# Kernel optimization log

Hardware: AMD Instinct MI355X
Metric: run time of the kernel (lower is better)

Reference implementation:

```python
import jax, jax.numpy as jnp
import numpy as np

B, N, D = 1, 1024, 3584
H, KVH, HD = 28, 4, 128
I = 18944
SEC = [16, 24, 24]  # mrope_section, sums to HD//2
EPS_RMS = 1e-6
EPS_SM = 1e-6


def setup_inputs() -> dict:
    key = jax.random.key(0)
    ks = jax.random.split(key, 16)
    s = 0.02
    return {
        "hidden_states": jax.random.normal(ks[0], (B, N, D), jnp.float32),
        "cos": jax.random.uniform(ks[1], (3, B, N, HD), jnp.float32, -1.0, 1.0),
        "sin": jax.random.uniform(ks[2], (3, B, N, HD), jnp.float32, -1.0, 1.0),
        "prune_mask": jax.random.randint(ks[3], (B, N), 0, 2, jnp.int32),
        "Wq": jax.random.normal(ks[4], (D, H * HD), jnp.float32) * s,
        "bq": jnp.zeros((H * HD,), jnp.float32),
        "Wk": jax.random.normal(ks[5], (D, KVH * HD), jnp.float32) * s,
        "bk": jnp.zeros((KVH * HD,), jnp.float32),
        "Wv": jax.random.normal(ks[6], (D, KVH * HD), jnp.float32) * s,
        "bv": jnp.zeros((KVH * HD,), jnp.float32),
        "Wo": jax.random.normal(ks[7], (H * HD, D), jnp.float32) * s,
        "ln1_w": jnp.ones((D,), jnp.float32),
        "ln2_w": jnp.ones((D,), jnp.float32),
        "Wg": jax.random.normal(ks[8], (D, I), jnp.float32) * s,
        "Wu": jax.random.normal(ks[9], (D, I), jnp.float32) * s,
        "Wd": jax.random.normal(ks[10], (I, D), jnp.float32) * s,
    }


def _rmsnorm(x, w):
    v = jnp.mean(x * x, axis=-1, keepdims=True)
    return x * jax.lax.rsqrt(v + EPS_RMS) * w


def _rotate_half(x):
    h = x.shape[-1] // 2
    return jnp.concatenate([-x[..., h:], x[..., :h]], axis=-1)


def _mrope_select(t):
    # t: (3, B, N, HD) -> (B, 1, N, HD), picking section i from axis i%3
    parts, idx = [], 0
    for i, s in enumerate(SEC * 2):
        parts.append(t[i % 3, :, :, idx:idx + s])
        idx += s
    return jnp.concatenate(parts, axis=-1)[:, None]


def reference(hidden_states, cos, sin, prune_mask, Wq, bq, Wk, bk, Wv, bv, Wo,
              ln1_w, ln2_w, Wg, Wu, Wd):
    x = _rmsnorm(hidden_states, ln1_w)
    q = (x @ Wq + bq).reshape(B, N, H, HD).transpose(0, 2, 1, 3)
    k = (x @ Wk + bk).reshape(B, N, KVH, HD).transpose(0, 2, 1, 3)
    v = (x @ Wv + bv).reshape(B, N, KVH, HD).transpose(0, 2, 1, 3)

    cf, sf = _mrope_select(cos), _mrope_select(sin)
    q = q * cf + _rotate_half(q) * sf
    k = k * cf + _rotate_half(k) * sf

    groups = H // KVH
    k = jnp.repeat(k, groups, axis=1)  # (B,H,N,HD)
    v = jnp.repeat(v, groups, axis=1)

    scores = jnp.einsum("bhqd,bhkd->bhqk", q, k) / np.sqrt(HD).astype(np.float32)
    causal = jnp.tril(jnp.ones((N, N), bool))
    scores = jnp.where(causal, scores, jnp.float32(-1e9))

    # custom prune-masked softmax (softmax_with_mask)
    am = prune_mask.astype(jnp.float32)[:, None, None, :]  # (B,1,1,N)
    eye = jnp.eye(N, dtype=jnp.float32)
    am = am + (1.0 - am) * eye
    mx = jnp.max(scores, axis=-1, keepdims=True)
    e = jnp.exp(scores - mx) * am
    attn = (e + EPS_SM / N) / (jnp.sum(e, axis=-1, keepdims=True) + EPS_SM)

    o = jnp.einsum("bhqk,bhkd->bhqd", attn, v)
    o = o.transpose(0, 2, 1, 3).reshape(B, N, H * HD) @ Wo

    h = hidden_states + o
    y = _rmsnorm(h, ln2_w)
    mlp = (jax.nn.silu(y @ Wg) * (y @ Wu)) @ Wd
    return h + mlp
```

## Files before the change

kernel.cpp:

```cpp
#include <hip/hip_runtime.h>
#include <hip/hip_bf16.h>


#define SEQ   1024
#define DIM   3584
#define NH    28
#define NKVH  4
#define HDIM  128
#define IDIM  18944
#define QKVN  4608
#define GUN   37888

typedef __attribute__((ext_vector_type(8))) __bf16 bf16x8;
typedef __attribute__((ext_vector_type(4))) __bf16 bf16x4;
typedef __attribute__((ext_vector_type(4))) float  f32x4;

static constexpr size_t OFF_WQKVT = 0;
static constexpr size_t OFF_WOT   = OFF_WQKVT + (size_t)QKVN*DIM*2;
static constexpr size_t OFF_WGUT  = OFF_WOT   + (size_t)DIM*DIM*2;
static constexpr size_t OFF_WDT   = OFF_WGUT  + (size_t)GUN*DIM*2;
static constexpr size_t OFF_XB    = OFF_WDT   + (size_t)DIM*IDIM*2;
static constexpr size_t OFF_QKV   = OFF_XB    + (size_t)SEQ*DIM*2;
static constexpr size_t OFF_VT    = OFF_QKV   + (size_t)SEQ*QKVN*2;
static constexpr size_t OFF_VSUMP = OFF_VT    + (size_t)NKVH*HDIM*SEQ*2;
static constexpr size_t OFF_VSUM  = OFF_VSUMP + 4*8*128*4;
static constexpr size_t OFF_BQKV  = OFF_VSUM  + 4*128*4;
static constexpr size_t OFF_OB    = OFF_BQKV  + (size_t)QKVN*4;
static constexpr size_t OFF_HB    = OFF_OB    + (size_t)SEQ*DIM*2;
static constexpr size_t OFF_YB    = OFF_HB    + (size_t)SEQ*DIM*4;
static constexpr size_t OFF_GU    = OFF_YB    + (size_t)SEQ*DIM*2;
static constexpr size_t OFF_PB    = OFF_GU    + (size_t)SEQ*GUN*2;
static constexpr size_t OFF_PART  = OFF_GU;

#define GLL16(gp, lp)                                                        \
  __builtin_amdgcn_global_load_lds(                                         \
      (const __attribute__((address_space(1))) void*)(gp),                  \
      (__attribute__((address_space(3))) void*)(lp), 16, 0, 0)

#define BAR    asm volatile("s_barrier" ::: "memory")
#define LGKM0  asm volatile("s_waitcnt lgkmcnt(0)" ::: "memory")
#define VM4    asm volatile("s_waitcnt vmcnt(4)" ::: "memory")

__global__ __launch_bounds__(256) void transconv_kernel(
    const float* __restrict__ W, __bf16* __restrict__ WT, int K, int N, int mode)
{
  __shared__ __bf16 t[64][72];
  const int tid = threadIdx.x;
  const int k0 = blockIdx.y * 64, n0 = blockIdx.x * 64;
#pragma unroll
  for (int it = 0; it < 4; ++it) {
    int idx = it * 256 + tid;
    int r = idx >> 4, c4 = idx & 15;
    float4 v = *(const float4*)(W + (size_t)(k0 + r) * N + n0 + c4 * 4);
    t[r][c4 * 4 + 0] = (__bf16)v.x;
    t[r][c4 * 4 + 1] = (__bf16)v.y;
    t[r][c4 * 4 + 2] = (__bf16)v.z;
    t[r][c4 * 4 + 3] = (__bf16)v.w;
  }
  __syncthreads();
#pragma unroll
  for (int it = 0; it < 2; ++it) {
    int idx = it * 256 + tid;
    int r = idx >> 3, c8 = idx & 7;
    bf16x8 o;
#pragma unroll
    for (int i = 0; i < 8; ++i) o[i] = t[c8 * 8 + i][r];
    const int nlog = n0 + r;
    const int orow = (mode == 0) ? nlog
                   : ((nlog >> 4) << 5) + ((mode == 2) ? 16 : 0) + (nlog & 15);
    *(bf16x8*)(WT + (size_t)orow * K + k0 + c8 * 8) = o;
  }
}

__global__ __launch_bounds__(256) void pack_bias_kernel(
    const float* __restrict__ bq, const float* __restrict__ bk,
    const float* __restrict__ bv, float* __restrict__ out)
{
  int i = blockIdx.x * 256 + threadIdx.x;
  if (i < DIM) out[i] = bq[i];
  else if (i < DIM + 512) out[i] = bk[i - DIM];
  else if (i < QKVN) out[i] = bv[i - DIM - 512];
}

__global__ __launch_bounds__(256) void rmsnorm_kernel(
    const float* __restrict__ in, const float* __restrict__ w,
    __bf16* __restrict__ out)
{
  const int row = blockIdx.x;
  const int t = threadIdx.x;
  const float* x = in + (size_t)row * DIM;
  float4 v[4];
  float ss = 0.f;
#pragma unroll
  for (int i = 0; i < 4; ++i) {
    int idx = t + i * 256;
    if (idx < 896) {
      v[i] = ((const float4*)x)[idx];
      ss += v[i].x * v[i].x + v[i].y * v[i].y + v[i].z * v[i].z + v[i].w * v[i].w;
    }
  }
#pragma unroll
  for (int m = 1; m < 64; m <<= 1) ss += __shfl_xor(ss, m);
  __shared__ float red[4];
  if ((t & 63) == 0) red[t >> 6] = ss;
  __syncthreads();
  float tot = red[0] + red[1] + red[2] + red[3];
  float rs = rsqrtf(tot / (float)DIM + 1e-6f);
#pragma unroll
  for (int i = 0; i < 4; ++i) {
    int idx = t + i * 256;
    if (idx < 896) {
      float4 wv = ((const float4*)w)[idx];
      bf16x4 o;
      o[0] = (__bf16)(v[i].x * rs * wv.x);
      o[1] = (__bf16)(v[i].y * rs * wv.y);
      o[2] = (__bf16)(v[i].z * rs * wv.z);
      o[3] = (__bf16)(v[i].w * rs * wv.w);
      *(bf16x4*)(out + (size_t)row * DIM + idx * 4) = o;
    }
  }
}

template<int S, bool BF16OUT, bool BIAS>
__global__ __launch_bounds__(256) void reduce_kernel(
    const float* __restrict__ part, const float* __restrict__ resid,
    const float* __restrict__ bias, void* __restrict__ out, int N, int MN4)
{
  const int i4 = blockIdx.x * 256 + threadIdx.x;
  if (i4 >= MN4) return;
  const size_t base = (size_t)i4 * 4;
  f32x4 s = *(const f32x4*)(part + base);
#pragma unroll
  for (int k = 1; k < S; ++k)
    s += *(const f32x4*)(part + (size_t)k * MN4 * 4 + base);
  if (BIAS) {
    const int col = (int)(base % N);
    s += *(const f32x4*)(bias + col);
  }
  if (resid != nullptr) s += *(const f32x4*)(resid + base);
  if (BF16OUT) {
    bf16x4 o;
#pragma unroll
    for (int j = 0; j < 4; ++j) o[j] = (__bf16)s[j];
    *(bf16x4*)((__bf16*)out + base) = o;
  } else {
    *(f32x4*)((float*)out + base) = s;
  }
}

template<int EPI>
__global__ __launch_bounds__(512, 1) void gemm256_kernel(
    const __bf16* __restrict__ A, const __bf16* __restrict__ BT,
    void* __restrict__ OUT, int M, int N, int K, int Kc, int gridY)
{
  __shared__ int4 lds4[8192];
  char* ldsc = (char*)lds4;
  const int tid = threadIdx.x;
  const int l = tid & 63, w = tid >> 6;
  const int wr = w >> 2, wc = w & 3;
  const int lg = l >> 4, lc = l & 15;

  const int nwg = gridDim.x;
  const int bq8 = nwg >> 3, br8 = nwg & 7;
  const int xcd = blockIdx.x & 7, bidx = blockIdx.x >> 3;
  const int wg = (xcd < br8 ? xcd * (bq8 + 1) : br8 * (bq8 + 1) + (xcd - br8) * bq8) + bidx;
  const int ntn = N >> 8;
  const int wg2 = wg / gridY;
  const int row0 = (wg % gridY) * 256;
  const int col0 = (wg2 % ntn) * 256;
  const int ks = wg2 / ntn;
  const int kbase = ks * Kc;

  size_t aoffj[2], boffj[2];
  int dstj[2];
#pragma unroll
  for (int j = 0; j < 2; ++j) {
    const int c = (j * 8 + w) * 64 + l;
    const int r = c >> 3, p = c & 7;
    const int b = p ^ (r & 7);
    aoffj[j] = (size_t)(row0 + r) * K + kbase + b * 8;
    boffj[j] = (size_t)(col0 + r) * K + kbase + b * 8;
    dstj[j] = (j * 8 + w) * 1024;
  }

#define STG_A(U, KT, BUFB) do {                                              \
    GLL16(A + aoffj[0] + (size_t)(U) * 128 * K + (size_t)(KT) * 64,          \
          ldsc + (BUFB) + (U) * 16384 + dstj[0]);                            \
    GLL16(A + aoffj[1] + (size_t)(U) * 128 * K + (size_t)(KT) * 64,          \
          ldsc + (BUFB) + (U) * 16384 + dstj[1]); } while (0)
#define STG_B(U, KT, BUFB) do {                                              \
    GLL16(BT + boffj[0] + (size_t)(U) * 128 * K + (size_t)(KT) * 64,         \
          ldsc + (BUFB) + 32768 + (U) * 16384 + dstj[0]);                    \
    GLL16(BT + boffj[1] + (size_t)(U) * 128 * K + (size_t)(KT) * 64,         \
          ldsc + (BUFB) + 32768 + (U) * 16384 + dstj[1]); } while (0)

  const int sw = lc & 7;
  const int rdA = (wr * 128 + lc) * 128;
  const int rdB = 32768 + (wc * 64 + lc) * 128;
  const int sk0 = (lg ^ sw) * 16;
  const int sk1 = ((4 | lg) ^ sw) * 16;

  f32x4 acc[8][4] = {};
  bf16x8 af[4][2], bfr[4][2];

#define RD_A4(MH, BUFB) do { _Pragma("unroll")                               \
    for (int mm = 0; mm < 4; ++mm) {                                         \
      af[mm][0] = *(const bf16x8*)(ldsc + (BUFB) + rdA + ((MH) * 4 + mm) * 2048 + sk0); \
      af[mm][1] = *(const bf16x8*)(ldsc + (BUFB) + rdA + ((MH) * 4 + mm) * 2048 + sk1); } } while (0)
#define RD_B2(NL, BUFB) do { _Pragma("unroll")                               \
    for (int nn = 0; nn < 2; ++nn) {                                         \
      bfr[(NL) + nn][0] = *(const bf16x8*)(ldsc + (BUFB) + rdB + ((NL) + nn) * 2048 + sk0); \
      bfr[(NL) + nn][1] = *(const bf16x8*)(ldsc + (BUFB) + rdB + ((NL) + nn) * 2048 + sk1); } } while (0)

#define MFMA16(MH, NL) do { _Pragma("unroll")                                \
    for (int mm = 0; mm < 4; ++mm) { _Pragma("unroll")                       \
      for (int nn = 0; nn < 2; ++nn) {                                       \
        acc[(MH)*4+mm][(NL)+nn] = __builtin_amdgcn_mfma_f32_16x16x32_bf16(   \
            af[mm][0], bfr[(NL)+nn][0], acc[(MH)*4+mm][(NL)+nn], 0, 0, 0);   \
        acc[(MH)*4+mm][(NL)+nn] = __builtin_amdgcn_mfma_f32_16x16x32_bf16(   \
            af[mm][1], bfr[(NL)+nn][1], acc[(MH)*4+mm][(NL)+nn], 0, 0, 0); } } } while (0)

#define DO_MFMA(MH, NL)                                                      \
    __builtin_amdgcn_s_setprio(1); MFMA16(MH, NL);                           \
    __builtin_amdgcn_s_setprio(0)

  STG_B(0, 0, 0); STG_B(1, 0, 0); STG_A(0, 0, 0); STG_A(1, 0, 0);
  STG_B(0, 1, 65536); STG_B(1, 1, 65536);
  VM4;
  BAR;

  const int T = Kc >> 6;
#pragma unroll 1
  for (int i = 0; i < (T >> 1); ++i) {
    const int t1 = 2 * i + 1;
    const int se = (2 * i + 2 < T) ? 2 * i + 2 : 2 * i;
    const int so = (2 * i + 3 < T) ? 2 * i + 3 : t1;
    RD_A4(0, 0); RD_B2(0, 0); STG_A(0, t1, 65536);
    BAR; LGKM0; DO_MFMA(0, 0); BAR;
    RD_B2(2, 0); STG_A(1, t1, 65536);
    BAR; LGKM0; DO_MFMA(0, 2); BAR;
    RD_A4(1, 0); STG_B(0, se, 0);
    BAR; LGKM0; DO_MFMA(1, 2); BAR;
    STG_B(1, se, 0);
    VM4;
    BAR; DO_MFMA(1, 0); BAR;
    RD_A4(0, 65536); RD_B2(0, 65536); STG_A(0, se, 0);
    BAR; LGKM0; DO_MFMA(0, 0); BAR;
    RD_B2(2, 65536); STG_A(1, se, 0);
    BAR; LGKM0; DO_MFMA(0, 2); BAR;
    RD_A4(1, 65536); STG_B(0, so, 65536);
    BAR; LGKM0; DO_MFMA(1, 2); BAR;
    STG_B(1, so, 65536);
    VM4;
    BAR; DO_MFMA(1, 0); BAR;
  }
  asm volatile("s_waitcnt vmcnt(0)" ::: "memory");

  if (EPI == 0) {
    __bf16* PBo = (__bf16*)OUT;
    const int id = N >> 1;
    const int baseq = (col0 + wc * 64) >> 5;
#pragma unroll
    for (int m = 0; m < 8; ++m) {
#pragma unroll
      for (int p = 0; p < 2; ++p) {
        const int gcol = (baseq + p) * 16 + lc;
#pragma unroll
        for (int j = 0; j < 4; ++j) {
          const int row = row0 + wr * 128 + m * 16 + lg * 4 + j;
          const float g = acc[m][2 * p][j];
          const float u = acc[m][2 * p + 1][j];
          const float s = g / (1.f + __expf(-g));
          PBo[(size_t)row * id + gcol] = (__bf16)(s * u);
        }
      }
    }
  } else {
    float* P = (float*)OUT + (size_t)ks * M * N;
#pragma unroll
    for (int m = 0; m < 8; ++m)
#pragma unroll
      for (int n = 0; n < 4; ++n)
#pragma unroll
        for (int j = 0; j < 4; ++j)
          P[(size_t)(row0 + wr * 128 + m * 16 + lg * 4 + j) * N
            + (col0 + wc * 64 + n * 16 + lc)] = acc[m][n][j];
  }
#undef STG_A
#undef STG_B
#undef RD_A4
#undef RD_B2
#undef MFMA16
#undef DO_MFMA
}

__global__ __launch_bounds__(256) void rope_kernel(
    __bf16* __restrict__ qkv, const float* __restrict__ cosb,
    const float* __restrict__ sinb)
{
  const int n = blockIdx.x;
  for (int p = threadIdx.x; p < 32 * 64; p += 256) {
    const int head = p >> 6;
    const int d = p & 63;
    const int src = (d < 16) ? 0 : (d < 40) ? 1 : 2;
    const float* cb = cosb + (size_t)src * SEQ * HDIM + (size_t)n * HDIM;
    const float* sb = sinb + (size_t)src * SEQ * HDIM + (size_t)n * HDIM;
    const float c0 = cb[d], c1 = cb[d + 64];
    const float s0 = sb[d], s1 = sb[d + 64];
    const int col = (head < NH) ? head * HDIM : DIM + (head - NH) * HDIM;
    __bf16* q = qkv + (size_t)n * QKVN + col;
    const float a = (float)q[d];
    const float b = (float)q[d + 64];
    q[d]      = (__bf16)(a * c0 - b * s0);
    q[d + 64] = (__bf16)(b * c1 + a * s1);
  }
}

__global__ __launch_bounds__(256) void vtrans_kernel(
    const __bf16* __restrict__ qkv, __bf16* __restrict__ vT,
    float* __restrict__ vsump)
{
  __shared__ __bf16 t[128][132];
  const int nt = blockIdx.x, kvh = blockIdx.y;
  const int n0 = nt * 128;
  const int tid = threadIdx.x;
#pragma unroll
  for (int it = 0; it < 8; ++it) {
    int idx = it * 256 + tid;
    int nl = idx >> 4, c8 = idx & 15;
    bf16x8 v = *(const bf16x8*)(qkv + (size_t)(n0 + nl) * QKVN + 4096 + kvh * HDIM + c8 * 8);
#pragma unroll
    for (int i = 0; i < 8; ++i) t[nl][c8 * 8 + i] = v[i];
  }
  __syncthreads();
#pragma unroll
  for (int it = 0; it < 8; ++it) {
    int idx = it * 256 + tid;
    int d = idx >> 4, c8 = idx & 15;
    bf16x8 o;
#pragma unroll
    for (int i = 0; i < 8; ++i) o[i] = t[c8 * 8 + i][d];
    *(bf16x8*)(vT + (size_t)(kvh * HDIM + d) * SEQ + n0 + c8 * 8) = o;
  }
  if (tid < 128) {
    float s = 0.f;
    for (int nl = 0; nl < 128; ++nl) s += (float)t[nl][tid];
    vsump[(size_t)(kvh * 8 + nt) * 128 + tid] = s;
  }
}

__global__ __launch_bounds__(512) void vsum_reduce_kernel(
    const float* __restrict__ vsump, float* __restrict__ vsum)
{
  const int idx = threadIdx.x;
  const int kvh = idx >> 7, d = idx & 127;
  float s = 0.f;
#pragma unroll
  for (int nt = 0; nt < 8; ++nt) s += vsump[(size_t)(kvh * 8 + nt) * 128 + d];
  vsum[idx] = s;
}

__global__ __launch_bounds__(256) void attn_kernel(
    const __bf16* __restrict__ qkv, const __bf16* __restrict__ vT,
    const float* __restrict__ vsum, const int* __restrict__ prune,
    __bf16* __restrict__ o)
{
  __shared__ __bf16 plds[4 * 16 * 40];
  const int tid = threadIdx.x;
  const int l = tid & 63, w = tid >> 6;
  const int h = blockIdx.y;
  const int kvh = h / 7;
  const int qt = blockIdx.x;
  const int qbase = qt * 64 + w * 16;
  const int lg = l >> 4, lc = l & 15;
  __bf16* pw = plds + w * (16 * 40);

  bf16x8 qf[4];
#pragma unroll
  for (int s = 0; s < 4; ++s)
    qf[s] = *(const bf16x8*)(qkv + (size_t)(qbase + lc) * QKVN + h * HDIM + s * 32 + lg * 8);

  f32x4 oacc[8] = {};
  float mrun[4] = {-3e38f, -3e38f, -3e38f, -3e38f};
  float lrun[4] = {0.f, 0.f, 0.f, 0.f};

  const int kbEnd = ((qbase + 15) >> 5) + 1;
  for (int kb = 0; kb < kbEnd; ++kb) {
    f32x4 sacc[2] = {};
#pragma unroll
    for (int s = 0; s < 4; ++s) {
#pragma unroll
      for (int c = 0; c < 2; ++c) {
        bf16x8 kf = *(const bf16x8*)(qkv + (size_t)(kb * 32 + c * 16 + lc) * QKVN
                                     + DIM + kvh * HDIM + s * 32 + lg * 8);
        sacc[c] = __builtin_amdgcn_mfma_f32_16x16x32_bf16(qf[s], kf, sacc[c], 0, 0, 0);
      }
    }
    float p[2][4];
    int am[2];
#pragma unroll
    for (int c = 0; c < 2; ++c) {
      const int col = kb * 32 + c * 16 + lc;
      am[c] = (prune[col] != 0) ? 1 : 0;
#pragma unroll
      for (int j = 0; j < 4; ++j) {
        const int row = qbase + lg * 4 + j;
        float sv = sacc[c][j] * 0.08838834764831845f;
        p[c][j] = (col <= row) ? sv : -3e38f;
      }
    }
#pragma unroll
    for (int j = 0; j < 4; ++j) {
      float mx = fmaxf(p[0][j], p[1][j]);
      mx = fmaxf(mx, __shfl_xor(mx, 1));
      mx = fmaxf(mx, __shfl_xor(mx, 2));
      mx = fmaxf(mx, __shfl_xor(mx, 4));
      mx = fmaxf(mx, __shfl_xor(mx, 8));
      const float mnew = fmaxf(mrun[j], mx);
      const float scale = __expf(mrun[j] - mnew);
      mrun[j] = mnew;
      const int row = qbase + lg * 4 + j;
      float rs = 0.f;
#pragma unroll
      for (int c = 0; c < 2; ++c) {
        const int col = kb * 32 + c * 16 + lc;
        float e = __expf(p[c][j] - mnew);
        const int keep = (col == row) ? 1 : am[c];
        e = keep ? e : 0.f;
        p[c][j] = e;
        rs += e;
      }
      rs += __shfl_xor(rs, 1);
      rs += __shfl_xor(rs, 2);
      rs += __shfl_xor(rs, 4);
      rs += __shfl_xor(rs, 8);
      lrun[j] = lrun[j] * scale + rs;
#pragma unroll
      for (int df = 0; df < 8; ++df) oacc[df][j] *= scale;
    }
#pragma unroll
    for (int c = 0; c < 2; ++c)
#pragma unroll
      for (int j = 0; j < 4; ++j)
        pw[(lg * 4 + j) * 40 + c * 16 + lc] = (__bf16)p[c][j];
    bf16x8 pa = *(const bf16x8*)(pw + lc * 40 + lg * 8);
#pragma unroll
    for (int df = 0; df < 8; ++df) {
      bf16x8 vf = *(const bf16x8*)(vT + (size_t)(kvh * HDIM + df * 16 + lc) * SEQ + kb * 32 + lg * 8);
      oacc[df] = __builtin_amdgcn_mfma_f32_16x16x32_bf16(pa, vf, oacc[df], 0, 0, 0);
    }
  }
#pragma unroll
  for (int df = 0; df < 8; ++df) {
    const float vs = vsum[kvh * HDIM + df * 16 + lc];
#pragma unroll
    for (int j = 0; j < 4; ++j) {
      const int row = qbase + lg * 4 + j;
      const float denom = lrun[j] + 1e-6f;
      const float val = (oacc[df][j] + 9.765625e-10f * vs) / denom;
      o[(size_t)row * DIM + h * HDIM + df * 16 + lc] = (__bf16)val;
    }
  }
}

extern "C" void kernel_launch(void* const* d_in, const int* in_sizes, int n_in,
                              void* d_out, int out_size, void* d_ws, size_t ws_size,
                              hipStream_t stream) {
  const float* hidden = (const float*)d_in[0];
  const float* cosb   = (const float*)d_in[1];
  const float* sinb   = (const float*)d_in[2];
  const int*   prune  = (const int*)d_in[3];
  const float* Wq     = (const float*)d_in[4];
  const float* bq     = (const float*)d_in[5];
  const float* Wk     = (const float*)d_in[6];
  const float* bk     = (const float*)d_in[7];
  const float* Wv     = (const float*)d_in[8];
  const float* bv     = (const float*)d_in[9];
  const float* Wo     = (const float*)d_in[10];
  const float* ln1    = (const float*)d_in[11];
  const float* ln2    = (const float*)d_in[12];
  const float* Wg     = (const float*)d_in[13];
  const float* Wu     = (const float*)d_in[14];
  const float* Wd     = (const float*)d_in[15];
  float* out = (float*)d_out;
  char* ws = (char*)d_ws;

  __bf16* WQKVT = (__bf16*)(ws + OFF_WQKVT);
  __bf16* WOT   = (__bf16*)(ws + OFF_WOT);
  __bf16* WGUT  = (__bf16*)(ws + OFF_WGUT);
  __bf16* WDT   = (__bf16*)(ws + OFF_WDT);
  __bf16* XB    = (__bf16*)(ws + OFF_XB);
  __bf16* QKV   = (__bf16*)(ws + OFF_QKV);
  __bf16* VT    = (__bf16*)(ws + OFF_VT);
  float*  VSUMP = (float*)(ws + OFF_VSUMP);
  float*  VSUM  = (float*)(ws + OFF_VSUM);
  float*  BQKV  = (float*)(ws + OFF_BQKV);
  __bf16* OB    = (__bf16*)(ws + OFF_OB);
  float*  HB    = (float*)(ws + OFF_HB);
  __bf16* YB    = (__bf16*)(ws + OFF_YB);
  __bf16* PB    = (__bf16*)(ws + OFF_PB);
  float*  PART  = (float*)(ws + OFF_PART);

  transconv_kernel<<<dim3(DIM / 64, DIM / 64), 256, 0, stream>>>(Wq, WQKVT, DIM, DIM, 0);
  transconv_kernel<<<dim3(512 / 64, DIM / 64), 256, 0, stream>>>(Wk, WQKVT + (size_t)DIM * DIM, DIM, 512, 0);
  transconv_kernel<<<dim3(512 / 64, DIM / 64), 256, 0, stream>>>(Wv, WQKVT + (size_t)4096 * DIM, DIM, 512, 0);
  pack_bias_kernel<<<QKVN / 256, 256, 0, stream>>>(bq, bk, bv, BQKV);
  rmsnorm_kernel<<<SEQ, 256, 0, stream>>>(hidden, ln1, XB);

  gemm256_kernel<1><<<(SEQ / 256) * (QKVN / 256) * 2, 512, 0, stream>>>(
      XB, WQKVT, PART, SEQ, QKVN, DIM, DIM / 2, SEQ / 256);
  reduce_kernel<2, true, true><<<(SEQ * QKVN / 4 + 255) / 256, 256, 0, stream>>>(
      PART, nullptr, BQKV, QKV, QKVN, SEQ * QKVN / 4);

  rope_kernel<<<SEQ, 256, 0, stream>>>(QKV, cosb, sinb);
  vtrans_kernel<<<dim3(8, NKVH), 256, 0, stream>>>(QKV, VT, VSUMP);
  vsum_reduce_kernel<<<1, 512, 0, stream>>>(VSUMP, VSUM);
  attn_kernel<<<dim3(SEQ / 64, NH), 256, 0, stream>>>(QKV, VT, VSUM, prune, OB);

  transconv_kernel<<<dim3(DIM / 64, DIM / 64), 256, 0, stream>>>(Wo, WOT, DIM, DIM, 0);
  gemm256_kernel<1><<<(DIM / 256) * (SEQ / 256) * 4, 512, 0, stream>>>(
      OB, WOT, PART, SEQ, DIM, DIM, DIM / 4, SEQ / 256);
  reduce_kernel<4, false, false><<<(SEQ * DIM / 4 + 255) / 256, 256, 0, stream>>>(
      PART, hidden, nullptr, HB, DIM, SEQ * DIM / 4);

  rmsnorm_kernel<<<SEQ, 256, 0, stream>>>(HB, ln2, YB);

  transconv_kernel<<<dim3(IDIM / 64, DIM / 64), 256, 0, stream>>>(Wg, WGUT, DIM, IDIM, 1);
  transconv_kernel<<<dim3(IDIM / 64, DIM / 64), 256, 0, stream>>>(Wu, WGUT, DIM, IDIM, 2);
  gemm256_kernel<0><<<(GUN / 256) * (SEQ / 256), 512, 0, stream>>>(
      YB, WGUT, PB, SEQ, GUN, DIM, DIM, SEQ / 256);

  transconv_kernel<<<dim3(DIM / 64, IDIM / 64), 256, 0, stream>>>(Wd, WDT, IDIM, DIM, 0);
  gemm256_kernel<1><<<(DIM / 256) * (SEQ / 256) * 4, 512, 0, stream>>>(
      PB, WDT, PART, SEQ, DIM, IDIM, IDIM / 4, SEQ / 256);
  reduce_kernel<4, false, false><<<(SEQ * DIM / 4 + 255) / 256, 256, 0, stream>>>(
      PART, HB, nullptr, out, DIM, SEQ * DIM / 4);
}
```

Before: 938.1 us.

## Switch GEMM to 32x32x16 MFMA tiles and fuse split-K reduce with RMSNorm

Changes the 256x256 GEMM inner loop from 16x16x32 MFMAs to 32x32x16 MFMAs. The fragment layout, LDS read pattern and both epilogues are reworked to match, and the SiLU*up pairing now uses a lane shuffle. Launch bounds are raised to allow two workgroups per CU. A new fused kernel sums the O-projection split-K partials with the residual, then computes RMSNorm and writes the bf16 output, replacing two separate kernels. The larger MFMA shape is meant to cut LDS reads per flop. The risks are register pressure under the new launch bound and less efficient strided epilogue stores.

```diff
diff --git a/kernel.cpp b/kernel.cpp
--- a/kernel.cpp
+++ b/kernel.cpp
@@ -11,9 +11,10 @@
 #define QKVN  4608
 #define GUN   37888
 
-typedef __attribute__((ext_vector_type(8))) __bf16 bf16x8;
-typedef __attribute__((ext_vector_type(4))) __bf16 bf16x4;
-typedef __attribute__((ext_vector_type(4))) float  f32x4;
+typedef __attribute__((ext_vector_type(8)))  __bf16 bf16x8;
+typedef __attribute__((ext_vector_type(4)))  __bf16 bf16x4;
+typedef __attribute__((ext_vector_type(4)))  float  f32x4;
+typedef __attribute__((ext_vector_type(16))) float  f32x16;
 
 static constexpr size_t OFF_WQKVT = 0;
 static constexpr size_t OFF_WOT   = OFF_WQKVT + (size_t)QKVN*DIM*2;
@@ -148,8 +149,53 @@
   }
 }
 
+__global__ __launch_bounds__(256) void reduce_rms_kernel(
+    const float* __restrict__ part, const float* __restrict__ resid,
+    const float* __restrict__ w, float* __restrict__ hout,
+    __bf16* __restrict__ yout)
+{
+  const int row = blockIdx.x;
+  const int t = threadIdx.x;
+  const size_t base = (size_t)row * DIM;
+  const size_t slab = (size_t)SEQ * DIM;
+  f32x4 v[4];
+  float ss = 0.f;
+#pragma unroll
+  for (int i = 0; i < 4; ++i) {
+    int idx = t + i * 256;
+    if (idx < 896) {
+      f32x4 s = *(const f32x4*)(part + base + idx * 4);
+      s += *(const f32x4*)(part + slab + base + idx * 4);
+      s += *(const f32x4*)(part + 2 * slab + base + idx * 4);
+      s += *(const f32x4*)(part + 3 * slab + base + idx * 4);
+      s += *(const f32x4*)(resid + base + idx * 4);
+      v[i] = s;
+      ss += s[0] * s[0] + s[1] * s[1] + s[2] * s[2] + s[3] * s[3];
+      *(f32x4*)(hout + base + idx * 4) = s;
+    }
+  }
+#pragma unroll
+  for (int m = 1; m < 64; m <<= 1) ss += __shfl_xor(ss, m);
+  __shared__ float red[4];
+  if ((t & 63) == 0) red[t >> 6] = ss;
+  __syncthreads();
+  float tot = red[0] + red[1] + red[2] + red[3];
+  float rs = rsqrtf(tot / (float)DIM + 1e-6f);
+#pragma unroll
+  for (int i = 0; i < 4; ++i) {
+    int idx = t + i * 256;
+    if (idx < 896) {
+      f32x4 wv = *(const f32x4*)(w + idx * 4);
+      bf16x4 o;
+#pragma unroll
+      for (int j = 0; j < 4; ++j) o[j] = (__bf16)(v[i][j] * rs * wv[j]);
+      *(bf16x4*)(yout + base + idx * 4) = o;
+    }
+  }
+}
+
 template<int EPI>
-__global__ __launch_bounds__(512, 1) void gemm256_kernel(
+__global__ __launch_bounds__(512, 2) void gemm256_kernel(
     const __bf16* __restrict__ A, const __bf16* __restrict__ BT,
     void* __restrict__ OUT, int M, int N, int K, int Kc, int gridY)
 {
@@ -158,7 +204,7 @@
   const int tid = threadIdx.x;
   const int l = tid & 63, w = tid >> 6;
   const int wr = w >> 2, wc = w & 3;
-  const int lg = l >> 4, lc = l & 15;
+  const int l31 = l & 31, oct = l >> 5;
 
   const int nwg = gridDim.x;
   const int bq8 = nwg >> 3, br8 = nwg & 7;
@@ -168,8 +214,8 @@
   const int wg2 = wg / gridY;
   const int row0 = (wg % gridY) * 256;
   const int col0 = (wg2 % ntn) * 256;
-  const int ks = wg2 / ntn;
-  const int kbase = ks * Kc;
+  const int ks_ = wg2 / ntn;
+  const int kbase = ks_ * Kc;
 
   size_t aoffj[2], boffj[2];
   int dstj[2];
@@ -194,34 +240,33 @@
     GLL16(BT + boffj[1] + (size_t)(U) * 128 * K + (size_t)(KT) * 64,         \
           ldsc + (BUFB) + 32768 + (U) * 16384 + dstj[1]); } while (0)
 
-  const int sw = lc & 7;
-  const int rdA = (wr * 128 + lc) * 128;
-  const int rdB = 32768 + (wc * 64 + lc) * 128;
-  const int sk0 = (lg ^ sw) * 16;
-  const int sk1 = ((4 | lg) ^ sw) * 16;
-
-  f32x4 acc[8][4] = {};
-  bf16x8 af[4][2], bfr[4][2];
-
-#define RD_A4(MH, BUFB) do { _Pragma("unroll")                               \
-    for (int mm = 0; mm < 4; ++mm) {                                         \
-      af[mm][0] = *(const bf16x8*)(ldsc + (BUFB) + rdA + ((MH) * 4 + mm) * 2048 + sk0); \
-      af[mm][1] = *(const bf16x8*)(ldsc + (BUFB) + rdA + ((MH) * 4 + mm) * 2048 + sk1); } } while (0)
-#define RD_B2(NL, BUFB) do { _Pragma("unroll")                               \
-    for (int nn = 0; nn < 2; ++nn) {                                         \
-      bfr[(NL) + nn][0] = *(const bf16x8*)(ldsc + (BUFB) + rdB + ((NL) + nn) * 2048 + sk0); \
-      bfr[(NL) + nn][1] = *(const bf16x8*)(ldsc + (BUFB) + rdB + ((NL) + nn) * 2048 + sk1); } } while (0)
-
-#define MFMA16(MH, NL) do { _Pragma("unroll")                                \
-    for (int mm = 0; mm < 4; ++mm) { _Pragma("unroll")                       \
-      for (int nn = 0; nn < 2; ++nn) {                                       \
-        acc[(MH)*4+mm][(NL)+nn] = __builtin_amdgcn_mfma_f32_16x16x32_bf16(   \
-            af[mm][0], bfr[(NL)+nn][0], acc[(MH)*4+mm][(NL)+nn], 0, 0, 0);   \
-        acc[(MH)*4+mm][(NL)+nn] = __builtin_amdgcn_mfma_f32_16x16x32_bf16(   \
-            af[mm][1], bfr[(NL)+nn][1], acc[(MH)*4+mm][(NL)+nn], 0, 0, 0); } } } while (0)
+  const int rbA = (wr * 128 + l31) * 128;
+  const int rbB = 32768 + (wc * 64 + l31) * 128;
+  int sk[4];
+#pragma unroll
+  for (int ks = 0; ks < 4; ++ks) sk[ks] = ((ks * 2 + oct) ^ (l & 7)) * 16;
+
+  f32x16 acc[4][2] = {};
+  bf16x8 af[2][4], bfr[2][4];
+
+#define RD_A2(MH, BUFB) do { _Pragma("unroll")                               \
+    for (int mm = 0; mm < 2; ++mm) { _Pragma("unroll")                       \
+      for (int ks = 0; ks < 4; ++ks)                                         \
+        af[mm][ks] = *(const bf16x8*)(ldsc + (BUFB) + rbA                    \
+            + ((MH) * 2 + mm) * 4096 + sk[ks]); } } while (0)
+#define RD_B4(NL, BUFB) do { _Pragma("unroll")                               \
+    for (int ks = 0; ks < 4; ++ks)                                           \
+      bfr[NL][ks] = *(const bf16x8*)(ldsc + (BUFB) + rbB                     \
+          + (NL) * 4096 + sk[ks]); } while (0)
+
+#define MFMA8(MH, NL) do { _Pragma("unroll")                                 \
+    for (int ks = 0; ks < 4; ++ks) { _Pragma("unroll")                       \
+      for (int mm = 0; mm < 2; ++mm)                                         \
+        acc[(MH)*2+mm][NL] = __builtin_amdgcn_mfma_f32_32x32x16_bf16(        \
+            af[mm][ks], bfr[NL][ks], acc[(MH)*2+mm][NL], 0, 0, 0); } } while (0)
 
 #define DO_MFMA(MH, NL)                                                      \
-    __builtin_amdgcn_s_setprio(1); MFMA16(MH, NL);                           \
+    __builtin_amdgcn_s_setprio(1); MFMA8(MH, NL);                            \
     __builtin_amdgcn_s_setprio(0)
 
   STG_B(0, 0, 0); STG_B(1, 0, 0); STG_A(0, 0, 0); STG_A(1, 0, 0);
@@ -233,64 +278,68 @@
 #pragma unroll 1
   for (int i = 0; i < (T >> 1); ++i) {
     const int t1 = 2 * i + 1;
-    const int se = (2 * i + 2 < T) ? 2 * i + 2 : 2 * i;
+    const int se = (2 * i + 2 < T) ? 2 * i + 2 : 0;
     const int so = (2 * i + 3 < T) ? 2 * i + 3 : t1;
-    RD_A4(0, 0); RD_B2(0, 0); STG_A(0, t1, 65536);
+    RD_A2(0, 0); RD_B4(0, 0); STG_A(0, t1, 65536);
     BAR; LGKM0; DO_MFMA(0, 0); BAR;
-    RD_B2(2, 0); STG_A(1, t1, 65536);
-    BAR; LGKM0; DO_MFMA(0, 2); BAR;
-    RD_A4(1, 0); STG_B(0, se, 0);
-    BAR; LGKM0; DO_MFMA(1, 2); BAR;
+    RD_B4(1, 0); STG_A(1, t1, 65536);
+    BAR; LGKM0; DO_MFMA(0, 1); BAR;
+    RD_A2(1, 0); STG_B(0, se, 0);
+    BAR; LGKM0; DO_MFMA(1, 0); BAR;
     STG_B(1, se, 0);
     VM4;
-    BAR; DO_MFMA(1, 0); BAR;
-    RD_A4(0, 65536); RD_B2(0, 65536); STG_A(0, se, 0);
+    BAR; DO_MFMA(1, 1); BAR;
+    RD_A2(0, 65536); RD_B4(0, 65536); STG_A(0, se, 0);
     BAR; LGKM0; DO_MFMA(0, 0); BAR;
-    RD_B2(2, 65536); STG_A(1, se, 0);
-    BAR; LGKM0; DO_MFMA(0, 2); BAR;
-    RD_A4(1, 65536); STG_B(0, so, 65536);
-    BAR; LGKM0; DO_MFMA(1, 2); BAR;
+    RD_B4(1, 65536); STG_A(1, se, 0);
+    BAR; LGKM0; DO_MFMA(0, 1); BAR;
+    RD_A2(1, 65536); STG_B(0, so, 65536);
+    BAR; LGKM0; DO_MFMA(1, 0); BAR;
     STG_B(1, so, 65536);
     VM4;
-    BAR; DO_MFMA(1, 0); BAR;
+    BAR; DO_MFMA(1, 1); BAR;
   }
   asm volatile("s_waitcnt vmcnt(0)" ::: "memory");
 
   if (EPI == 0) {
     __bf16* PBo = (__bf16*)OUT;
     const int id = N >> 1;
-    const int baseq = (col0 + wc * 64) >> 5;
-#pragma unroll
-    for (int m = 0; m < 8; ++m) {
-#pragma unroll
-      for (int p = 0; p < 2; ++p) {
-        const int gcol = (baseq + p) * 16 + lc;
-#pragma unroll
-        for (int j = 0; j < 4; ++j) {
-          const int row = row0 + wr * 128 + m * 16 + lg * 4 + j;
-          const float g = acc[m][2 * p][j];
-          const float u = acc[m][2 * p + 1][j];
-          const float s = g / (1.f + __expf(-g));
-          PBo[(size_t)row * id + gcol] = (__bf16)(s * u);
+#pragma unroll
+    for (int m = 0; m < 4; ++m) {
+#pragma unroll
+      for (int n = 0; n < 2; ++n) {
+        const int q = (col0 + wc * 64 + n * 32) >> 5;
+#pragma unroll
+        for (int reg = 0; reg < 16; ++reg) {
+          const int row = row0 + wr * 128 + m * 32
+                        + (reg & 3) + 8 * (reg >> 2) + 4 * oct;
+          const float g = acc[m][n][reg];
+          const float u = __shfl_xor(g, 16);
+          if (l31 < 16) {
+            const float s = g / (1.f + __expf(-g));
+            PBo[(size_t)row * id + q * 16 + (l & 15)] = (__bf16)(s * u);
+          }
         }
       }
     }
   } else {
-    float* P = (float*)OUT + (size_t)ks * M * N;
-#pragma unroll
-    for (int m = 0; m < 8; ++m)
-#pragma unroll
-      for (int n = 0; n < 4; ++n)
-#pragma unroll
-        for (int j = 0; j < 4; ++j)
-          P[(size_t)(row0 + wr * 128 + m * 16 + lg * 4 + j) * N
-            + (col0 + wc * 64 + n * 16 + lc)] = acc[m][n][j];
+    float* P = (float*)OUT + (size_t)ks_ * M * N;
+#pragma unroll
+    for (int m = 0; m < 4; ++m)
+#pragma unroll
+      for (int n = 0; n < 2; ++n)
+#pragma unroll
+        for (int reg = 0; reg < 16; ++reg) {
+          const int row = row0 + wr * 128 + m * 32
+                        + (reg & 3) + 8 * (reg >> 2) + 4 * oct;
+          P[(size_t)row * N + col0 + wc * 64 + n * 32 + l31] = acc[m][n][reg];
+        }
   }
 #undef STG_A
 #undef STG_B
-#undef RD_A4
-#undef RD_B2
-#undef MFMA16
+#undef RD_A2
+#undef RD_B4
+#undef MFMA8
 #undef DO_MFMA
 }
 
@@ -520,10 +569,7 @@
   transconv_kernel<<<dim3(DIM / 64, DIM / 64), 256, 0, stream>>>(Wo, WOT, DIM, DIM, 0);
   gemm256_kernel<1><<<(DIM / 256) * (SEQ / 256) * 4, 512, 0, stream>>>(
       OB, WOT, PART, SEQ, DIM, DIM, DIM / 4, SEQ / 256);
-  reduce_kernel<4, false, false><<<(SEQ * DIM / 4 + 255) / 256, 256, 0, stream>>>(
-      PART, hidden, nullptr, HB, DIM, SEQ * DIM / 4);
-
-  rmsnorm_kernel<<<SEQ, 256, 0, stream>>>(HB, ln2, YB);
+  reduce_rms_kernel<<<SEQ, 256, 0, stream>>>(PART, hidden, ln2, HB, YB);
 
   transconv_kernel<<<dim3(IDIM / 64, DIM / 64), 256, 0, stream>>>(Wg, WGUT, DIM, IDIM, 1);
   transconv_kernel<<<dim3(IDIM / 64, DIM / 64), 256, 0, stream>>>(Wu, WGUT, DIM, IDIM, 2);
```

Measured after the change: 1.021 ms. +8.8%, slower.

## Persist gate/up GEMM with atomic tile scheduler and fuse reduce with RMSNorm

Applied to the files above, without the earlier changes.

The gate/up GEMM now runs as a persistent kernel with 256 workgroups that take 256x256 output tiles from a global atomic counter. Before, it launched one workgroup per tile. The counter is reset inside a new fused kernel that sums the O-projection split-K partials, adds the residual, and applies the second RMSNorm in one pass, replacing a separate reduce and a separate rmsnorm launch. The goal is to cut the tail-wave imbalance across 592 tiles and save one launch plus one read and write of HB. The cost is an atomic and a barrier per tile, and the loss of the XCD-aware tile ordering in the persistent path, which may reduce L2 locality.

```diff
diff --git a/kernel.cpp b/kernel.cpp
--- a/kernel.cpp
+++ b/kernel.cpp
@@ -31,6 +31,7 @@
 static constexpr size_t OFF_GU    = OFF_YB    + (size_t)SEQ*DIM*2;
 static constexpr size_t OFF_PB    = OFF_GU    + (size_t)SEQ*GUN*2;
 static constexpr size_t OFF_PART  = OFF_GU;
+static constexpr size_t OFF_CTR   = OFF_VSUMP;
 
 #define GLL16(gp, lp)                                                        \
   __builtin_amdgcn_global_load_lds(                                         \
@@ -148,40 +149,108 @@
   }
 }
 
-template<int EPI>
+__global__ __launch_bounds__(256) void reduce_rms_kernel(
+    const float* __restrict__ part, const float* __restrict__ resid,
+    const float* __restrict__ w, float* __restrict__ hout,
+    __bf16* __restrict__ yout, int* __restrict__ ctr)
+{
+  const int row = blockIdx.x;
+  const int t = threadIdx.x;
+  if (row == 0 && t == 0) atomicExch(ctr, 0);
+  const size_t base = (size_t)row * DIM;
+  const size_t slab = (size_t)SEQ * DIM;
+  f32x4 v[4];
+  float ss = 0.f;
+#pragma unroll
+  for (int i = 0; i < 4; ++i) {
+    int idx = t + i * 256;
+    if (idx < 896) {
+      f32x4 s = *(const f32x4*)(part + base + idx * 4);
+      s += *(const f32x4*)(part + slab + base + idx * 4);
+      s += *(const f32x4*)(part + 2 * slab + base + idx * 4);
+      s += *(const f32x4*)(part + 3 * slab + base + idx * 4);
+      s += *(const f32x4*)(resid + base + idx * 4);
+      v[i] = s;
+      ss += s[0] * s[0] + s[1] * s[1] + s[2] * s[2] + s[3] * s[3];
+      *(f32x4*)(hout + base + idx * 4) = s;
+    }
+  }
+#pragma unroll
+  for (int m = 1; m < 64; m <<= 1) ss += __shfl_xor(ss, m);
+  __shared__ float red[4];
+  if ((t & 63) == 0) red[t >> 6] = ss;
+  __syncthreads();
+  float tot = red[0] + red[1] + red[2] + red[3];
+  float rs = rsqrtf(tot / (float)DIM + 1e-6f);
+#pragma unroll
+  for (int i = 0; i < 4; ++i) {
+    int idx = t + i * 256;
+    if (idx < 896) {
+      f32x4 wv = *(const f32x4*)(w + idx * 4);
+      bf16x4 o;
+#pragma unroll
+      for (int j = 0; j < 4; ++j) o[j] = (__bf16)(v[i][j] * rs * wv[j]);
+      *(bf16x4*)(yout + base + idx * 4) = o;
+    }
+  }
+}
+
+template<int EPI, int PERSIST>
 __global__ __launch_bounds__(512, 1) void gemm256_kernel(
     const __bf16* __restrict__ A, const __bf16* __restrict__ BT,
-    void* __restrict__ OUT, int M, int N, int K, int Kc, int gridY)
+    void* __restrict__ OUT, int M, int N, int K, int Kc, int gridY,
+    int NT, int* __restrict__ ctr)
 {
   __shared__ int4 lds4[8192];
+  __shared__ int s_t;
   char* ldsc = (char*)lds4;
   const int tid = threadIdx.x;
   const int l = tid & 63, w = tid >> 6;
   const int wr = w >> 2, wc = w & 3;
   const int lg = l >> 4, lc = l & 15;
 
-  const int nwg = gridDim.x;
-  const int bq8 = nwg >> 3, br8 = nwg & 7;
-  const int xcd = blockIdx.x & 7, bidx = blockIdx.x >> 3;
-  const int wg = (xcd < br8 ? xcd * (bq8 + 1) : br8 * (bq8 + 1) + (xcd - br8) * bq8) + bidx;
-  const int ntn = N >> 8;
-  const int wg2 = wg / gridY;
-  const int row0 = (wg % gridY) * 256;
-  const int col0 = (wg2 % ntn) * 256;
-  const int ks = wg2 / ntn;
-  const int kbase = ks * Kc;
-
-  size_t aoffj[2], boffj[2];
-  int dstj[2];
+  int cdst[2], crow[2], cslot[2];
 #pragma unroll
   for (int j = 0; j < 2; ++j) {
     const int c = (j * 8 + w) * 64 + l;
-    const int r = c >> 3, p = c & 7;
-    const int b = p ^ (r & 7);
-    aoffj[j] = (size_t)(row0 + r) * K + kbase + b * 8;
-    boffj[j] = (size_t)(col0 + r) * K + kbase + b * 8;
-    dstj[j] = (j * 8 + w) * 1024;
-  }
+    crow[j] = c >> 3;
+    cslot[j] = (c & 7) ^ (crow[j] & 7);
+    cdst[j] = (j * 8 + w) * 1024;
+  }
+  const int sw = lc & 7;
+  const int rdA = (wr * 128 + lc) * 128;
+  const int rdB = 32768 + (wc * 64 + lc) * 128;
+  const int sk0 = (lg ^ sw) * 16;
+  const int sk1 = ((4 | lg) ^ sw) * 16;
+  const int ntn = N >> 8;
+
+  for (;;) {
+    int tw;
+    if (PERSIST) {
+      if (tid == 0) s_t = atomicAdd(ctr, 1);
+      __syncthreads();
+      tw = s_t;
+      if (tw >= NT) return;
+    } else {
+      const int nwg = gridDim.x;
+      const int bq8 = nwg >> 3, br8 = nwg & 7;
+      const int xcd = blockIdx.x & 7, bidx = blockIdx.x >> 3;
+      tw = (xcd < br8 ? xcd * (bq8 + 1) : br8 * (bq8 + 1) + (xcd - br8) * bq8) + bidx;
+    }
+    const int wg2 = tw / gridY;
+    const int row0 = (tw % gridY) * 256;
+    const int col0 = (wg2 % ntn) * 256;
+    const int ks_ = wg2 / ntn;
+    const int kbase = ks_ * Kc;
+
+    size_t aoffj[2], boffj[2];
+    int dstj[2];
+#pragma unroll
+    for (int j = 0; j < 2; ++j) {
+      aoffj[j] = (size_t)(row0 + crow[j]) * K + kbase + cslot[j] * 8;
+      boffj[j] = (size_t)(col0 + crow[j]) * K + kbase + cslot[j] * 8;
+      dstj[j] = cdst[j];
+    }
 
 #define STG_A(U, KT, BUFB) do {                                              \
     GLL16(A + aoffj[0] + (size_t)(U) * 128 * K + (size_t)(KT) * 64,          \
@@ -194,14 +263,8 @@
     GLL16(BT + boffj[1] + (size_t)(U) * 128 * K + (size_t)(KT) * 64,         \
           ldsc + (BUFB) + 32768 + (U) * 16384 + dstj[1]); } while (0)
 
-  const int sw = lc & 7;
-  const int rdA = (wr * 128 + lc) * 128;
-  const int rdB = 32768 + (wc * 64 + lc) * 128;
-  const int sk0 = (lg ^ sw) * 16;
-  const int sk1 = ((4 | lg) ^ sw) * 16;
-
-  f32x4 acc[8][4] = {};
-  bf16x8 af[4][2], bfr[4][2];
+    f32x4 acc[8][4] = {};
+    bf16x8 af[4][2], bfr[4][2];
 
 #define RD_A4(MH, BUFB) do { _Pragma("unroll")                               \
     for (int mm = 0; mm < 4; ++mm) {                                         \
@@ -224,67 +287,69 @@
     __builtin_amdgcn_s_setprio(1); MFMA16(MH, NL);                           \
     __builtin_amdgcn_s_setprio(0)
 
-  STG_B(0, 0, 0); STG_B(1, 0, 0); STG_A(0, 0, 0); STG_A(1, 0, 0);
-  STG_B(0, 1, 65536); STG_B(1, 1, 65536);
-  VM4;
-  BAR;
-
-  const int T = Kc >> 6;
+    STG_B(0, 0, 0); STG_B(1, 0, 0); STG_A(0, 0, 0); STG_A(1, 0, 0);
+    STG_B(0, 1, 65536); STG_B(1, 1, 65536);
+    VM4;
+    BAR;
+
+    const int T = Kc >> 6;
 #pragma unroll 1
-  for (int i = 0; i < (T >> 1); ++i) {
-    const int t1 = 2 * i + 1;
-    const int se = (2 * i + 2 < T) ? 2 * i + 2 : 2 * i;
-    const int so = (2 * i + 3 < T) ? 2 * i + 3 : t1;
-    RD_A4(0, 0); RD_B2(0, 0); STG_A(0, t1, 65536);
-    BAR; LGKM0; DO_MFMA(0, 0); BAR;
-    RD_B2(2, 0); STG_A(1, t1, 65536);
-    BAR; LGKM0; DO_MFMA(0, 2); BAR;
-    RD_A4(1, 0); STG_B(0, se, 0);
-    BAR; LGKM0; DO_MFMA(1, 2); BAR;
-    STG_B(1, se, 0);
-    VM4;
-    BAR; DO_MFMA(1, 0); BAR;
-    RD_A4(0, 65536); RD_B2(0, 65536); STG_A(0, se, 0);
-    BAR; LGKM0; DO_MFMA(0, 0); BAR;
-    RD_B2(2, 65536); STG_A(1, se, 0);
-    BAR; LGKM0; DO_MFMA(0, 2); BAR;
-    RD_A4(1, 65536); STG_B(0, so, 65536);
-    BAR; LGKM0; DO_MFMA(1, 2); BAR;
-    STG_B(1, so, 65536);
-    VM4;
-    BAR; DO_MFMA(1, 0); BAR;
-  }
-  asm volatile("s_waitcnt vmcnt(0)" ::: "memory");
-
-  if (EPI == 0) {
-    __bf16* PBo = (__bf16*)OUT;
-    const int id = N >> 1;
-    const int baseq = (col0 + wc * 64) >> 5;
-#pragma unroll
-    for (int m = 0; m < 8; ++m) {
-#pragma unroll
-      for (int p = 0; p < 2; ++p) {
-        const int gcol = (baseq + p) * 16 + lc;
-#pragma unroll
-        for (int j = 0; j < 4; ++j) {
-          const int row = row0 + wr * 128 + m * 16 + lg * 4 + j;
-          const float g = acc[m][2 * p][j];
-          const float u = acc[m][2 * p + 1][j];
-          const float s = g / (1.f + __expf(-g));
-          PBo[(size_t)row * id + gcol] = (__bf16)(s * u);
+    for (int i = 0; i < (T >> 1); ++i) {
+      const int t1 = 2 * i + 1;
+      const int se = (2 * i + 2 < T) ? 2 * i + 2 : 2 * i;
+      const int so = (2 * i + 3 < T) ? 2 * i + 3 : t1;
+      RD_A4(0, 0); RD_B2(0, 0); STG_A(0, t1, 65536);
+      BAR; LGKM0; DO_MFMA(0, 0); BAR;
+      RD_B2(2, 0); STG_A(1, t1, 65536);
+      BAR; LGKM0; DO_MFMA(0, 2); BAR;
+      RD_A4(1, 0); STG_B(0, se, 0);
+      BAR; LGKM0; DO_MFMA(1, 2); BAR;
+      STG_B(1, se, 0);
+      VM4;
+      BAR; DO_MFMA(1, 0); BAR;
+      RD_A4(0, 65536); RD_B2(0, 65536); STG_A(0, se, 0);
+      BAR; LGKM0; DO_MFMA(0, 0); BAR;
+      RD_B2(2, 65536); STG_A(1, se, 0);
+      BAR; LGKM0; DO_MFMA(0, 2); BAR;
+      RD_A4(1, 65536); STG_B(0, so, 65536);
+      BAR; LGKM0; DO_MFMA(1, 2); BAR;
+      STG_B(1, so, 65536);
+      VM4;
+      BAR; DO_MFMA(1, 0); BAR;
+    }
+    asm volatile("s_waitcnt vmcnt(0)" ::: "memory");
+
+    if (EPI == 0) {
+      __bf16* PBo = (__bf16*)OUT;
+      const int id = N >> 1;
+      const int baseq = (col0 + wc * 64) >> 5;
+#pragma unroll
+      for (int m = 0; m < 8; ++m) {
+#pragma unroll
+        for (int p = 0; p < 2; ++p) {
+          const int gcol = (baseq + p) * 16 + lc;
+#pragma unroll
+          for (int j = 0; j < 4; ++j) {
+            const int row = row0 + wr * 128 + m * 16 + lg * 4 + j;
+            const float g = acc[m][2 * p][j];
+            const float u = acc[m][2 * p + 1][j];
+            const float s = g / (1.f + __expf(-g));
+            PBo[(size_t)row * id + gcol] = (__bf16)(s * u);
+          }
         }
       }
-    }
-  } else {
-    float* P = (float*)OUT + (size_t)ks * M * N;
-#pragma unroll
-    for (int m = 0; m < 8; ++m)
-#pragma unroll
-      for (int n = 0; n < 4; ++n)
-#pragma unroll
-        for (int j = 0; j < 4; ++j)
-          P[(size_t)(row0 + wr * 128 + m * 16 + lg * 4 + j) * N
-            + (col0 + wc * 64 + n * 16 + lc)] = acc[m][n][j];
+    } else {
+      float* P = (float*)OUT + (size_t)ks_ * M * N;
+#pragma unroll
+      for (int m = 0; m < 8; ++m)
+#pragma unroll
+        for (int n = 0; n < 4; ++n)
+#pragma unroll
+          for (int j = 0; j < 4; ++j)
+            P[(size_t)(row0 + wr * 128 + m * 16 + lg * 4 + j) * N
+              + (col0 + wc * 64 + n * 16 + lc)] = acc[m][n][j];
+    }
+    if (!PERSIST) return;
   }
 #undef STG_A
 #undef STG_B
@@ -500,6 +565,7 @@
   __bf16* YB    = (__bf16*)(ws + OFF_YB);
   __bf16* PB    = (__bf16*)(ws + OFF_PB);
   float*  PART  = (float*)(ws + OFF_PART);
+  int*    CTR   = (int*)(ws + OFF_CTR);
 
   transconv_kernel<<<dim3(DIM / 64, DIM / 64), 256, 0, stream>>>(Wq, WQKVT, DIM, DIM, 0);
   transconv_kernel<<<dim3(512 / 64, DIM / 64), 256, 0, stream>>>(Wk, WQKVT + (size_t)DIM * DIM, DIM, 512, 0);
@@ -507,8 +573,8 @@
   pack_bias_kernel<<<QKVN / 256, 256, 0, stream>>>(bq, bk, bv, BQKV);
   rmsnorm_kernel<<<SEQ, 256, 0, stream>>>(hidden, ln1, XB);
 
-  gemm256_kernel<1><<<(SEQ / 256) * (QKVN / 256) * 2, 512, 0, stream>>>(
-      XB, WQKVT, PART, SEQ, QKVN, DIM, DIM / 2, SEQ / 256);
+  gemm256_kernel<1, 0><<<(SEQ / 256) * (QKVN / 256) * 2, 512, 0, stream>>>(
+      XB, WQKVT, PART, SEQ, QKVN, DIM, DIM / 2, SEQ / 256, 0, nullptr);
   reduce_kernel<2, true, true><<<(SEQ * QKVN / 4 + 255) / 256, 256, 0, stream>>>(
       PART, nullptr, BQKV, QKV, QKVN, SEQ * QKVN / 4);
 
@@ -518,21 +584,19 @@
   attn_kernel<<<dim3(SEQ / 64, NH), 256, 0, stream>>>(QKV, VT, VSUM, prune, OB);
 
   transconv_kernel<<<dim3(DIM / 64, DIM / 64), 256, 0, stream>>>(Wo, WOT, DIM, DIM, 0);
-  gemm256_kernel<1><<<(DIM / 256) * (SEQ / 256) * 4, 512, 0, stream>>>(
-      OB, WOT, PART, SEQ, DIM, DIM, DIM / 4, SEQ / 256);
-  reduce_kernel<4, false, false><<<(SEQ * DIM / 4 + 255) / 256, 256, 0, stream>>>(
-      PART, hidden, nullptr, HB, DIM, SEQ * DIM / 4);
-
-  rmsnorm_kernel<<<SEQ, 256, 0, stream>>>(HB, ln2, YB);
+  gemm256_kernel<1, 0><<<(DIM / 256) * (SEQ / 256) * 4, 512, 0, stream>>>(
+      OB, WOT, PART, SEQ, DIM, DIM, DIM / 4, SEQ / 256, 0, nullptr);
+  reduce_rms_kernel<<<SEQ, 256, 0, stream>>>(PART, hidden, ln2, HB, YB, CTR);
 
   transconv_kernel<<<dim3(IDIM / 64, DIM / 64), 256, 0, stream>>>(Wg, WGUT, DIM, IDIM, 1);
   transconv_kernel<<<dim3(IDIM / 64, DIM / 64), 256, 0, stream>>>(Wu, WGUT, DIM, IDIM, 2);
-  gemm256_kernel<0><<<(GUN / 256) * (SEQ / 256), 512, 0, stream>>>(
-      YB, WGUT, PB, SEQ, GUN, DIM, DIM, SEQ / 256);
+  gemm256_kernel<0, 1><<<256, 512, 0, stream>>>(
+      YB, WGUT, PB, SEQ, GUN, DIM, DIM, SEQ / 256,
+      (GUN / 256) * (SEQ / 256), CTR);
 
   transconv_kernel<<<dim3(DIM / 64, IDIM / 64), 256, 0, stream>>>(Wd, WDT, IDIM, DIM, 0);
-  gemm256_kernel<1><<<(DIM / 256) * (SEQ / 256) * 4, 512, 0, stream>>>(
-      PB, WDT, PART, SEQ, DIM, IDIM, IDIM / 4, SEQ / 256);
+  gemm256_kernel<1, 0><<<(DIM / 256) * (SEQ / 256) * 4, 512, 0, stream>>>(
+      PB, WDT, PART, SEQ, DIM, IDIM, IDIM / 4, SEQ / 256, 0, nullptr);
   reduce_kernel<4, false, false><<<(SEQ * DIM / 4 + 255) / 256, 256, 0, stream>>>(
       PART, HB, nullptr, out, DIM, SEQ * DIM / 4);
 }
```

After: 989.0 us. +5.4%, slower.
